# Kernel tuning notes

Measured on AMD Instinct MI355X. Metric: run time of the kernel, lower is better.

Reference implementation:

```python
import jax, jax.numpy as jnp
import numpy as np

VOCAB, EMBED, HIDDEN, NUM_OUT = 50000, 256, 64, 16
BATCH, T = 64, 2048
BN_EPS = 1e-5


def setup_inputs() -> dict:
    key = jax.random.key(0)
    ks = jax.random.split(key, 12)
    x = jax.random.randint(ks[0], (BATCH, T), 0, VOCAB, dtype=jnp.int64)
    seq_lengths = jax.random.randint(ks[1], (BATCH,), 1, T, dtype=jnp.int64)
    emb = jax.random.normal(ks[2], (VOCAB, EMBED), dtype=jnp.float32) * 0.1
    emb = emb.at[0].set(0.0)  # padding_idx=0
    s_ih = 1.0 / np.sqrt(HIDDEN)
    W_ih = jax.random.uniform(ks[3], (4 * HIDDEN, EMBED), jnp.float32, -s_ih, s_ih)
    W_hh = jax.random.uniform(ks[4], (4 * HIDDEN, HIDDEN), jnp.float32, -s_ih, s_ih)
    b_ih = jax.random.uniform(ks[5], (4 * HIDDEN,), jnp.float32, -s_ih, s_ih)
    b_hh = jax.random.uniform(ks[6], (4 * HIDDEN,), jnp.float32, -s_ih, s_ih)
    bn_gamma = jnp.ones((HIDDEN,), jnp.float32)
    bn_beta = jnp.zeros((HIDDEN,), jnp.float32)
    bn_mean = jnp.zeros((HIDDEN,), jnp.float32)
    bn_var = jnp.ones((HIDDEN,), jnp.float32)
    s_fc = 1.0 / np.sqrt(HIDDEN)
    fc_w = jax.random.uniform(ks[7], (NUM_OUT, HIDDEN), jnp.float32, -s_fc, s_fc)
    fc_b = jax.random.uniform(ks[8], (NUM_OUT,), jnp.float32, -s_fc, s_fc)
    return {"x": x, "seq_lengths": seq_lengths, "emb": emb, "W_ih": W_ih,
            "W_hh": W_hh, "b_ih": b_ih, "b_hh": b_hh, "bn_gamma": bn_gamma,
            "bn_beta": bn_beta, "bn_mean": bn_mean, "bn_var": bn_var,
            "fc_w": fc_w, "fc_b": fc_b}


def reference(x, seq_lengths, emb, W_ih, W_hh, b_ih, b_hh,
              bn_gamma, bn_beta, bn_mean, bn_var, fc_w, fc_b):
    B, Tn = x.shape
    H = W_hh.shape[1]
    x_embed = emb[x]                       # [B, T, E] (dropout is identity in eval)
    xe_t = jnp.transpose(x_embed, (1, 0, 2))  # [T, B, E] time-major for scan
    # precompute input projections for all timesteps in one big GEMM
    gx = jnp.einsum('tbe,ge->tbg', xe_t, W_ih) + b_ih + b_hh  # [T, B, 4H]

    def step(carry, gxt):
        h, c = carry
        gates = gxt + h @ W_hh.T           # [B, 4H]
        i, f, g, o = jnp.split(gates, 4, axis=-1)  # torch LSTMCell gate order
        i = jax.nn.sigmoid(i)
        f = jax.nn.sigmoid(f)
        g = jnp.tanh(g)
        o = jax.nn.sigmoid(o)
        c = f * c + i * g
        h = o * jnp.tanh(c)
        return (h, c), None

    h0 = jnp.zeros((B, H), x_embed.dtype)
    c0 = jnp.zeros((B, H), x_embed.dtype)
    (h_last, _), _ = jax.lax.scan(step, (h0, c0), gx)
    # BatchNorm1d (eval mode: running stats)
    h_bn = (h_last - bn_mean) * jax.lax.rsqrt(bn_var + BN_EPS) * bn_gamma + bn_beta
    return h_bn @ fc_w.T + fc_b            # [B, num_output]
```

## Files before the change

### kernel.cpp

```cpp
#include <hip/hip_runtime.h>
#include <math.h>

#define VOCAB   50000
#define EMBED   256
#define HIDDEN  64
#define G4      256
#define BATCH   64
#define TSEQ    2048
#define NUM_OUT 16

typedef _Float16 h2    __attribute__((ext_vector_type(2)));
typedef _Float16 f16x8 __attribute__((ext_vector_type(8)));
typedef float    f32x4 __attribute__((ext_vector_type(4)));

#define LOG2E  1.4426950408889634f
#define LOG2E2 2.8853900817779268f

__device__ __forceinline__ float fexp2f(float x) { return __builtin_amdgcn_exp2f(x); }
__device__ __forceinline__ float frcpf(float x)  { return __builtin_amdgcn_rcpf(x); }

__device__ __forceinline__ float dot2(h2 a, h2 b, float c) {
#if __has_builtin(__builtin_amdgcn_fdot2)
    return __builtin_amdgcn_fdot2(a, b, c, false);
#else
    float r;
    asm("v_dot2_f32_f16 %0, %1, %2, %3"
        : "=v"(r)
        : "v"(__builtin_bit_cast(int, a)), "v"(__builtin_bit_cast(int, b)), "v"(c));
    return r;
#endif
}

template <int CTRL>
__device__ __forceinline__ float dppf(float v) {
    return __int_as_float(__builtin_amdgcn_update_dpp(
        0, __float_as_int(v), CTRL, 0xF, 0xF, true));
}

#define REP32(M) M(0) M(1) M(2) M(3) M(4) M(5) M(6) M(7) \
                 M(8) M(9) M(10) M(11) M(12) M(13) M(14) M(15) \
                 M(16) M(17) M(18) M(19) M(20) M(21) M(22) M(23) \
                 M(24) M(25) M(26) M(27) M(28) M(29) M(30) M(31)

__device__ __align__(16) short g_Wf16[G4 * EMBED];

__global__ __launch_bounds__(256) void wcvt_kernel(const float* __restrict__ W_ih) {
    int i = (blockIdx.x * 256 + threadIdx.x) * 4;
    float4 v = *(const float4*)&W_ih[i];
    short4 o;
    o.x = __builtin_bit_cast(short, (_Float16)v.x);
    o.y = __builtin_bit_cast(short, (_Float16)v.y);
    o.z = __builtin_bit_cast(short, (_Float16)v.z);
    o.w = __builtin_bit_cast(short, (_Float16)v.w);
    *(short4*)&g_Wf16[i] = o;
}

__global__ __launch_bounds__(256) void proj_mfma(
    const float* __restrict__ emb,
    const float* __restrict__ b_ih, const float* __restrict__ b_hh,
    float* __restrict__ proj)
{
    __shared__ __align__(16) short As[64][264];

    const int tid  = threadIdx.x;
    const int w    = tid >> 6;
    const int lane = tid & 63;
    const int R0   = blockIdx.x * 64;

    #pragma unroll
    for (int it = 0; it < 16; ++it) {
        int flat = it * 256 + tid;
        int r  = flat >> 6;
        int c4 = flat & 63;
        int row = R0 + r; row = row < VOCAB ? row : VOCAB - 1;
        float4 v = *(const float4*)&emb[(size_t)row * EMBED + c4 * 4];
        short4 o;
        o.x = __builtin_bit_cast(short, (_Float16)v.x);
        o.y = __builtin_bit_cast(short, (_Float16)v.y);
        o.z = __builtin_bit_cast(short, (_Float16)v.z);
        o.w = __builtin_bit_cast(short, (_Float16)v.w);
        *(short4*)&As[r][c4 * 4] = o;
    }
    __syncthreads();

    f32x4 acc[16];
    #pragma unroll
    for (int t = 0; t < 16; ++t) acc[t] = f32x4{0.f, 0.f, 0.f, 0.f};

    const short* arow = &As[w * 16 + (lane & 15)][(lane >> 4) * 8];
    const int boff = (lane & 15) * EMBED + (lane >> 4) * 8;

    #pragma unroll
    for (int kc = 0; kc < 8; ++kc) {
        f16x8 af = *(const f16x8*)(arow + kc * 32);
        #pragma unroll
        for (int t = 0; t < 16; ++t) {
            f16x8 bf = *(const f16x8*)&g_Wf16[t * 16 * EMBED + kc * 32 + boff];
            acc[t] = __builtin_amdgcn_mfma_f32_16x16x32_f16(af, bf, acc[t], 0, 0, 0);
        }
    }

    const int crow0 = R0 + w * 16 + (lane >> 4) * 4;
    const int colin = lane & 15;
    #pragma unroll
    for (int t = 0; t < 16; ++t) {
        int g = t * 16 + colin;
        float bias = b_ih[g] + b_hh[g];
        float sc = ((g >> 6) == 2) ? LOG2E2 : LOG2E;
        #pragma unroll
        for (int j = 0; j < 4; ++j) {
            int row = crow0 + j;
            if (row < VOCAB)
                proj[(size_t)row * G4 + g] = (acc[t][j] + bias) * sc;
        }
    }
}

__global__ __launch_bounds__(256) void lstm_scan(
    const int* __restrict__ x, const float* __restrict__ proj,
    const float* __restrict__ W_hh,
    const float* __restrict__ bn_gamma, const float* __restrict__ bn_beta,
    const float* __restrict__ bn_mean, const float* __restrict__ bn_var,
    const float* __restrict__ fc_w, const float* __restrict__ fc_b,
    float* __restrict__ out)
{
    const int b   = blockIdx.x;
    const int tid = threadIdx.x;
    const int w   = tid >> 6;
    const int l   = tid & 63;
    const int q   = l & 3;
    const int unit = w * 16 + (l >> 2);

    __shared__ int   toks[TSEQ + 8];
    __shared__ __align__(16) short hbuf[2][HIDDEN];
    __shared__ float hfin[HIDDEN];
    __shared__ float hb_s[HIDDEN];

    for (int i = tid; i < TSEQ + 8; i += 256)
        toks[i] = x[b * TSEQ + (i < TSEQ ? i : TSEQ - 1)];
    if (tid < 2 * HIDDEN) ((short*)hbuf)[tid] = 0;

    const float s_k = (q == 2) ? LOG2E2 : LOG2E;
    const float* Wr = &W_hh[(size_t)(q * HIDDEN + unit) * HIDDEN];
#define WR_DECL(n) h2 wr##n;
    REP32(WR_DECL)
#undef WR_DECL
#define WR_LOAD(n) { float2 v = *(const float2*)&Wr[2 * (n)]; \
                     wr##n = h2{(_Float16)(v.x * s_k), (_Float16)(v.y * s_k)}; }
    REP32(WR_LOAD)
#undef WR_LOAD

    const float s_c = (q == 2) ? LOG2E2 : 1.0f;
    const float s_m = (q == 2) ? 2.0f * LOG2E2 : 1.0f;
    const bool qodd = (q & 1) != 0;
    const bool qhi  = (q & 2) != 0;

    float c = 0.0f, hmy = 0.0f;
    const float* projw = proj + q * HIDDEN + unit;

    __syncthreads();

    float gx0 = projw[(size_t)toks[0] * G4];
    float gx1 = projw[(size_t)toks[1] * G4];
    float gx2 = projw[(size_t)toks[2] * G4];
    float gx3 = projw[(size_t)toks[3] * G4];
    int tk0 = toks[4], tk1 = toks[5], tk2 = toks[6], tk3 = toks[7];

    const int4* hp0 = (const int4*)hbuf[0];
    const int4* hp1 = (const int4*)hbuf[1];

#define DOTG(R, W0, W1, W2, W3) \
    a0 = dot2(W0, __builtin_bit_cast(h2, R.x), a0); \
    a1 = dot2(W1, __builtin_bit_cast(h2, R.y), a1); \
    a2 = dot2(W2, __builtin_bit_cast(h2, R.z), a2); \
    a3 = dot2(W3, __builtin_bit_cast(h2, R.w), a3);

#define STEP(HP, WB, GX, TK, TT) { \
    int4 r0 = (HP)[0], r1 = (HP)[1], r2 = (HP)[2], r3 = (HP)[3]; \
    int4 r4 = (HP)[4], r5 = (HP)[5], r6 = (HP)[6], r7 = (HP)[7]; \
    int tnew = toks[(TT) + 8]; \
    float gnew = projw[(size_t)(TK) * G4]; \
    float a0 = GX, a1 = 0.f, a2 = 0.f, a3 = 0.f; \
    DOTG(r0, wr0,  wr1,  wr2,  wr3)  DOTG(r1, wr4,  wr5,  wr6,  wr7) \
    DOTG(r2, wr8,  wr9,  wr10, wr11) DOTG(r3, wr12, wr13, wr14, wr15) \
    DOTG(r4, wr16, wr17, wr18, wr19) DOTG(r5, wr20, wr21, wr22, wr23) \
    DOTG(r6, wr24, wr25, wr26, wr27) DOTG(r7, wr28, wr29, wr30, wr31) \
    float gv = (a0 + a1) + (a2 + a3); \
    GX = gnew; TK = tnew; \
    float tt2 = fexp2f(gv); \
    float rr = fmaf(-s_m, frcpf(tt2 + 1.0f), s_c);        \
    float b1 = dppf<0xB1>(rr);                            \
    float b2 = dppf<0x4E>(rr);                            \
    float b3 = dppf<0x1B>(rr);                            \
    float A  = qodd ? b1 : rr,  B  = qodd ? b3 : b2; \
    float A2 = qodd ? rr : b1,  B2 = qodd ? b2 : b3; \
    float i_ = qhi ? B  : A,    g_ = qhi ? A  : B; \
    float f_ = qhi ? B2 : A2,   o_ = qhi ? A2 : B2; \
    float o2 = o_ + o_; \
    c = fmaf(f_, c, i_ * g_);                             \
    float e2 = fexp2f(c); \
    float rv = frcpf(e2 + 1.0f); \
    hmy = fmaf(-o2, rv, o_);                              \
    if (q == 0) hbuf[WB][unit] = __builtin_bit_cast(short, (_Float16)hmy); \
    asm volatile("s_waitcnt lgkmcnt(0)" ::: "memory"); \
    __builtin_amdgcn_s_barrier(); \
    asm volatile("" ::: "memory"); \
}

    for (int t = 0; t < TSEQ; t += 4) {
        STEP(hp0, 1, gx0, tk0, t)
        STEP(hp1, 0, gx1, tk1, t + 1)
        STEP(hp0, 1, gx2, tk2, t + 2)
        STEP(hp1, 0, gx3, tk3, t + 3)
    }
#undef STEP
#undef DOTG

    if (q == 0) hfin[unit] = hmy;
    __syncthreads();
    if (tid < HIDDEN) {
        float hb = (hfin[tid] - bn_mean[tid]) * rsqrtf(bn_var[tid] + 1e-5f)
                   * bn_gamma[tid] + bn_beta[tid];
        hb_s[tid] = hb;
    }
    __syncthreads();
    if (tid < NUM_OUT) {
        float s0 = fc_b[tid], s1 = 0.f, s2 = 0.f, s3 = 0.f;
        #pragma unroll
        for (int k = 0; k < HIDDEN; k += 4) {
            s0 = fmaf(hb_s[k + 0], fc_w[tid * HIDDEN + k + 0], s0);
            s1 = fmaf(hb_s[k + 1], fc_w[tid * HIDDEN + k + 1], s1);
            s2 = fmaf(hb_s[k + 2], fc_w[tid * HIDDEN + k + 2], s2);
            s3 = fmaf(hb_s[k + 3], fc_w[tid * HIDDEN + k + 3], s3);
        }
        out[b * NUM_OUT + tid] = (s0 + s1) + (s2 + s3);
    }
}

extern "C" void kernel_launch(void* const* d_in, const int* in_sizes, int n_in,
                              void* d_out, int out_size, void* d_ws, size_t ws_size,
                              hipStream_t stream) {
    const int*   x        = (const int*)d_in[0];
    const float* emb      = (const float*)d_in[2];
    const float* W_ih     = (const float*)d_in[3];
    const float* W_hh     = (const float*)d_in[4];
    const float* b_ih     = (const float*)d_in[5];
    const float* b_hh     = (const float*)d_in[6];
    const float* bn_gamma = (const float*)d_in[7];
    const float* bn_beta  = (const float*)d_in[8];
    const float* bn_mean  = (const float*)d_in[9];
    const float* bn_var   = (const float*)d_in[10];
    const float* fc_w     = (const float*)d_in[11];
    const float* fc_b     = (const float*)d_in[12];

    float* proj = (float*)d_ws;

    wcvt_kernel<<<G4 * EMBED / (256 * 4), 256, 0, stream>>>(W_ih);
    proj_mfma<<<(VOCAB + 63) / 64, 256, 0, stream>>>(emb, b_ih, b_hh, proj);

    lstm_scan<<<BATCH, 256, 0, stream>>>(x, proj, W_hh,
                                         bn_gamma, bn_beta, bn_mean, bn_var,
                                         fc_w, fc_b, (float*)d_out);
}
```

Baseline: 642.6 us.

## Run LSTM recurrence in a single wavefront using MFMA for the hidden matmul

The per-batch scan kernel moves from 256 threads with fp16 dot2 products and a block barrier every step to a single 64-lane wavefront. That wavefront computes h·W_hh^T with 16x16x32 MFMA instructions, W_hh is kept in registers as f16 B fragments, and h is exchanged through a small shared buffer with no s_barrier. The projection table layout is permuted so each lane can fetch its 16 gate inputs with four float4 loads, and the projection kernel writes vectorized float4 stores. The aim is to remove the cross-wave barrier cost and the latency of the dot-product chain on the serial critical path. In exchange, most MFMA output is wasted because only row 0 is used, and each lane must compute 16 activations per step.

```diff
diff --git a/kernel.cpp b/kernel.cpp
--- a/kernel.cpp
+++ b/kernel.cpp
@@ -9,7 +9,6 @@
 #define TSEQ    2048
 #define NUM_OUT 16
 
-typedef _Float16 h2    __attribute__((ext_vector_type(2)));
 typedef _Float16 f16x8 __attribute__((ext_vector_type(8)));
 typedef float    f32x4 __attribute__((ext_vector_type(4)));
 
@@ -19,28 +18,17 @@
 __device__ __forceinline__ float fexp2f(float x) { return __builtin_amdgcn_exp2f(x); }
 __device__ __forceinline__ float frcpf(float x)  { return __builtin_amdgcn_rcpf(x); }
 
-__device__ __forceinline__ float dot2(h2 a, h2 b, float c) {
-#if __has_builtin(__builtin_amdgcn_fdot2)
-    return __builtin_amdgcn_fdot2(a, b, c, false);
-#else
-    float r;
-    asm("v_dot2_f32_f16 %0, %1, %2, %3"
-        : "=v"(r)
-        : "v"(__builtin_bit_cast(int, a)), "v"(__builtin_bit_cast(int, b)), "v"(c));
-    return r;
-#endif
-}
-
-template <int CTRL>
-__device__ __forceinline__ float dppf(float v) {
-    return __int_as_float(__builtin_amdgcn_update_dpp(
-        0, __float_as_int(v), CTRL, 0xF, 0xF, true));
-}
-
-#define REP32(M) M(0) M(1) M(2) M(3) M(4) M(5) M(6) M(7) \
-                 M(8) M(9) M(10) M(11) M(12) M(13) M(14) M(15) \
-                 M(16) M(17) M(18) M(19) M(20) M(21) M(22) M(23) \
-                 M(24) M(25) M(26) M(27) M(28) M(29) M(30) M(31)
+__device__ __forceinline__ int dpp_xor1(int v) {
+    return __builtin_amdgcn_update_dpp(0, v, 0xB1, 0xF, 0xF, true);
+}
+__device__ __forceinline__ int pkpair(float h) {
+    int hp = dpp_xor1(__float_as_int(h));
+    return __builtin_bit_cast(int,
+        __builtin_amdgcn_cvt_pkrtz(h, __int_as_float(hp)));
+}
+
+#define REP16(M) M(0) M(1) M(2) M(3) M(4) M(5) M(6) M(7) \
+                 M(8) M(9) M(10) M(11) M(12) M(13) M(14) M(15)
 
 __device__ __align__(16) short g_Wf16[G4 * EMBED];
 
@@ -102,21 +90,33 @@
 
     const int crow0 = R0 + w * 16 + (lane >> 4) * 4;
     const int colin = lane & 15;
+
+    float bs[16], sc[16];
     #pragma unroll
     for (int t = 0; t < 16; ++t) {
         int g = t * 16 + colin;
-        float bias = b_ih[g] + b_hh[g];
-        float sc = ((g >> 6) == 2) ? LOG2E2 : LOG2E;
-        #pragma unroll
-        for (int j = 0; j < 4; ++j) {
-            int row = crow0 + j;
-            if (row < VOCAB)
-                proj[(size_t)row * G4 + g] = (acc[t][j] + bias) * sc;
-        }
-    }
-}
-
-__global__ __launch_bounds__(256) void lstm_scan(
+        bs[t] = b_ih[g] + b_hh[g];
+        sc[t] = ((t >> 2) == 2) ? LOG2E2 : LOG2E;
+    }
+
+    #pragma unroll
+    for (int j = 0; j < 4; ++j) {
+        int row = crow0 + j;
+        if (row < VOCAB) {
+            #pragma unroll
+            for (int a = 0; a < 4; ++a) {
+                float4 o;
+                o.x = (acc[4 * a + 0][j] + bs[4 * a + 0]) * sc[4 * a + 0];
+                o.y = (acc[4 * a + 1][j] + bs[4 * a + 1]) * sc[4 * a + 1];
+                o.z = (acc[4 * a + 2][j] + bs[4 * a + 2]) * sc[4 * a + 2];
+                o.w = (acc[4 * a + 3][j] + bs[4 * a + 3]) * sc[4 * a + 3];
+                *(float4*)&proj[(size_t)row * G4 + colin * 16 + 4 * a] = o;
+            }
+        }
+    }
+}
+
+__global__ __launch_bounds__(64, 1) void lstm_scan(
     const int* __restrict__ x, const float* __restrict__ proj,
     const float* __restrict__ W_hh,
     const float* __restrict__ bn_gamma, const float* __restrict__ bn_beta,
@@ -124,116 +124,134 @@
     const float* __restrict__ fc_w, const float* __restrict__ fc_b,
     float* __restrict__ out)
 {
-    const int b   = blockIdx.x;
-    const int tid = threadIdx.x;
-    const int w   = tid >> 6;
-    const int l   = tid & 63;
-    const int q   = l & 3;
-    const int unit = w * 16 + (l >> 2);
-
-    __shared__ int   toks[TSEQ + 8];
-    __shared__ __align__(16) short hbuf[2][HIDDEN];
-    __shared__ float hfin[HIDDEN];
+    const int b    = blockIdx.x;
+    const int lane = threadIdx.x;
+    const int g    = lane >> 4;
+    const int c    = lane & 15;
+
+    __shared__ int   toks[TSEQ + 4];
+    __shared__ __align__(16) int hx[32];
     __shared__ float hb_s[HIDDEN];
 
-    for (int i = tid; i < TSEQ + 8; i += 256)
+    for (int i = lane; i < TSEQ + 4; i += 64)
         toks[i] = x[b * TSEQ + (i < TSEQ ? i : TSEQ - 1)];
-    if (tid < 2 * HIDDEN) ((short*)hbuf)[tid] = 0;
-
-    const float s_k = (q == 2) ? LOG2E2 : LOG2E;
-    const float* Wr = &W_hh[(size_t)(q * HIDDEN + unit) * HIDDEN];
-#define WR_DECL(n) h2 wr##n;
-    REP32(WR_DECL)
-#undef WR_DECL
-#define WR_LOAD(n) { float2 v = *(const float2*)&Wr[2 * (n)]; \
-                     wr##n = h2{(_Float16)(v.x * s_k), (_Float16)(v.y * s_k)}; }
-    REP32(WR_LOAD)
-#undef WR_LOAD
-
-    const float s_c = (q == 2) ? LOG2E2 : 1.0f;
-    const float s_m = (q == 2) ? 2.0f * LOG2E2 : 1.0f;
-    const bool qodd = (q & 1) != 0;
-    const bool qhi  = (q & 2) != 0;
-
-    float c = 0.0f, hmy = 0.0f;
-    const float* projw = proj + q * HIDDEN + unit;
-
-    __syncthreads();
-
-    float gx0 = projw[(size_t)toks[0] * G4];
-    float gx1 = projw[(size_t)toks[1] * G4];
-    float gx2 = projw[(size_t)toks[2] * G4];
-    float gx3 = projw[(size_t)toks[3] * G4];
-    int tk0 = toks[4], tk1 = toks[5], tk2 = toks[6], tk3 = toks[7];
-
-    const int4* hp0 = (const int4*)hbuf[0];
-    const int4* hp1 = (const int4*)hbuf[1];
-
-#define DOTG(R, W0, W1, W2, W3) \
-    a0 = dot2(W0, __builtin_bit_cast(h2, R.x), a0); \
-    a1 = dot2(W1, __builtin_bit_cast(h2, R.y), a1); \
-    a2 = dot2(W2, __builtin_bit_cast(h2, R.z), a2); \
-    a3 = dot2(W3, __builtin_bit_cast(h2, R.w), a3);
-
-#define STEP(HP, WB, GX, TK, TT) { \
-    int4 r0 = (HP)[0], r1 = (HP)[1], r2 = (HP)[2], r3 = (HP)[3]; \
-    int4 r4 = (HP)[4], r5 = (HP)[5], r6 = (HP)[6], r7 = (HP)[7]; \
-    int tnew = toks[(TT) + 8]; \
-    float gnew = projw[(size_t)(TK) * G4]; \
-    float a0 = GX, a1 = 0.f, a2 = 0.f, a3 = 0.f; \
-    DOTG(r0, wr0,  wr1,  wr2,  wr3)  DOTG(r1, wr4,  wr5,  wr6,  wr7) \
-    DOTG(r2, wr8,  wr9,  wr10, wr11) DOTG(r3, wr12, wr13, wr14, wr15) \
-    DOTG(r4, wr16, wr17, wr18, wr19) DOTG(r5, wr20, wr21, wr22, wr23) \
-    DOTG(r6, wr24, wr25, wr26, wr27) DOTG(r7, wr28, wr29, wr30, wr31) \
-    float gv = (a0 + a1) + (a2 + a3); \
-    GX = gnew; TK = tnew; \
-    float tt2 = fexp2f(gv); \
-    float rr = fmaf(-s_m, frcpf(tt2 + 1.0f), s_c);        \
-    float b1 = dppf<0xB1>(rr);                            \
-    float b2 = dppf<0x4E>(rr);                            \
-    float b3 = dppf<0x1B>(rr);                            \
-    float A  = qodd ? b1 : rr,  B  = qodd ? b3 : b2; \
-    float A2 = qodd ? rr : b1,  B2 = qodd ? b2 : b3; \
-    float i_ = qhi ? B  : A,    g_ = qhi ? A  : B; \
-    float f_ = qhi ? B2 : A2,   o_ = qhi ? A2 : B2; \
-    float o2 = o_ + o_; \
-    c = fmaf(f_, c, i_ * g_);                             \
-    float e2 = fexp2f(c); \
-    float rv = frcpf(e2 + 1.0f); \
-    hmy = fmaf(-o2, rv, o_);                              \
-    if (q == 0) hbuf[WB][unit] = __builtin_bit_cast(short, (_Float16)hmy); \
-    asm volatile("s_waitcnt lgkmcnt(0)" ::: "memory"); \
-    __builtin_amdgcn_s_barrier(); \
-    asm volatile("" ::: "memory"); \
-}
-
-    for (int t = 0; t < TSEQ; t += 4) {
-        STEP(hp0, 1, gx0, tk0, t)
-        STEP(hp1, 0, gx1, tk1, t + 1)
-        STEP(hp0, 1, gx2, tk2, t + 2)
-        STEP(hp1, 0, gx3, tk3, t + 3)
+    if (lane < 32) hx[lane] = 0;
+
+#define BDECL(t) f16x8 Ba##t, Bb##t;
+    REP16(BDECL)
+#undef BDECL
+#define BLOAD(t) { \
+        const float* wr = W_hh + (size_t)(t * 16 + c) * HIDDEN + g * 8; \
+        const float sck = ((t >> 2) == 2) ? LOG2E2 : LOG2E; \
+        float4 lo = *(const float4*)wr; \
+        float4 hi = *(const float4*)(wr + 4); \
+        Ba##t = f16x8{(_Float16)(lo.x*sck), (_Float16)(lo.y*sck), \
+                      (_Float16)(lo.z*sck), (_Float16)(lo.w*sck), \
+                      (_Float16)(hi.x*sck), (_Float16)(hi.y*sck), \
+                      (_Float16)(hi.z*sck), (_Float16)(hi.w*sck)}; \
+        lo = *(const float4*)(wr + 32); \
+        hi = *(const float4*)(wr + 36); \
+        Bb##t = f16x8{(_Float16)(lo.x*sck), (_Float16)(lo.y*sck), \
+                      (_Float16)(lo.z*sck), (_Float16)(lo.w*sck), \
+                      (_Float16)(hi.x*sck), (_Float16)(hi.y*sck), \
+                      (_Float16)(hi.z*sck), (_Float16)(hi.w*sck)}; }
+    REP16(BLOAD)
+#undef BLOAD
+
+    float cc0 = 0.f, cc1 = 0.f, cc2 = 0.f, cc3 = 0.f;
+    float hs0 = 0.f, hs1 = 0.f, hs2 = 0.f, hs3 = 0.f;
+
+    const float* projc = proj + c * 16;
+
+    const float4* gp0 = (const float4*)(projc + (size_t)toks[0] * G4);
+    const float4* gp1 = (const float4*)(projc + (size_t)toks[1] * G4);
+    float4 P0 = gp0[0], P1 = gp0[1], P2 = gp0[2], P3 = gp0[3];
+    float4 R0 = gp1[0], R1 = gp1[1], R2 = gp1[2], R3 = gp1[3];
+
+#define STEP(Q0, Q1, Q2, Q3, TT) { \
+    const int4* hx4 = (const int4*)hx; \
+    int4 a0i = hx4[g]; \
+    int4 a1i = hx4[4 + g]; \
+    f16x8 A0 = __builtin_bit_cast(f16x8, a0i); \
+    f16x8 A1 = __builtin_bit_cast(f16x8, a1i); \
+    int tk = toks[(TT) + 2]; \
+    const float4* gp = (const float4*)(projc + (size_t)tk * G4); \
+    float4 n0 = gp[0], n1 = gp[1], n2 = gp[2], n3 = gp[3]; \
+    float gxv[16]; \
+    gxv[0]=Q0.x; gxv[1]=Q0.y; gxv[2]=Q0.z; gxv[3]=Q0.w; \
+    gxv[4]=Q1.x; gxv[5]=Q1.y; gxv[6]=Q1.z; gxv[7]=Q1.w; \
+    gxv[8]=Q2.x; gxv[9]=Q2.y; gxv[10]=Q2.z; gxv[11]=Q2.w; \
+    gxv[12]=Q3.x; gxv[13]=Q3.y; gxv[14]=Q3.z; gxv[15]=Q3.w; \
+    const f32x4 zz = {0.f, 0.f, 0.f, 0.f}; \
+    MFMAS(A0, A1, zz) \
+    ACTS() \
+    UPD(0, r0, r4, r8,  r12) \
+    UPD(1, r1, r5, r9,  r13) \
+    UPD(2, r2, r6, r10, r14) \
+    UPD(3, r3, r7, r11, r15) \
+    int pk0 = pkpair(hs0), pk1 = pkpair(hs1); \
+    int pk2 = pkpair(hs2), pk3 = pkpair(hs3); \
+    if ((lane & 0x31) == 0) { \
+        int bi = c >> 1; \
+        hx[bi] = pk0; hx[8 + bi] = pk1; \
+        hx[16 + bi] = pk2; hx[24 + bi] = pk3; \
+    } \
+    Q0 = n0; Q1 = n1; Q2 = n2; Q3 = n3; \
+}
+#define MFMA1(t, A0, A1, ZZ) \
+    f32x4 ac##t = __builtin_amdgcn_mfma_f32_16x16x32_f16(A0, Ba##t, ZZ, 0, 0, 0); \
+    ac##t = __builtin_amdgcn_mfma_f32_16x16x32_f16(A1, Bb##t, ac##t, 0, 0, 0);
+#define MFMAS(A0, A1, ZZ) \
+    MFMA1(0,A0,A1,ZZ)  MFMA1(1,A0,A1,ZZ)  MFMA1(2,A0,A1,ZZ)  MFMA1(3,A0,A1,ZZ) \
+    MFMA1(4,A0,A1,ZZ)  MFMA1(5,A0,A1,ZZ)  MFMA1(6,A0,A1,ZZ)  MFMA1(7,A0,A1,ZZ) \
+    MFMA1(8,A0,A1,ZZ)  MFMA1(9,A0,A1,ZZ)  MFMA1(10,A0,A1,ZZ) MFMA1(11,A0,A1,ZZ) \
+    MFMA1(12,A0,A1,ZZ) MFMA1(13,A0,A1,ZZ) MFMA1(14,A0,A1,ZZ) MFMA1(15,A0,A1,ZZ)
+#define ACT1(t) float r##t; { \
+    float gv = ac##t[0] + gxv[t]; \
+    float e  = fexp2f(gv); \
+    float rv = frcpf(e + 1.0f); \
+    r##t = ((t) >> 2) == 2 ? fmaf(-2.0f * LOG2E2, rv, LOG2E2) \
+                           : fmaf(-1.0f, rv, 1.0f); }
+#define ACTS() \
+    ACT1(0)  ACT1(1)  ACT1(2)  ACT1(3)  ACT1(4)  ACT1(5)  ACT1(6)  ACT1(7) \
+    ACT1(8)  ACT1(9)  ACT1(10) ACT1(11) ACT1(12) ACT1(13) ACT1(14) ACT1(15)
+#define UPD(s, RI, RF, RG, RO) { \
+    cc##s = fmaf(RF, cc##s, RI * RG); \
+    float e2 = fexp2f(cc##s); \
+    float rv2 = frcpf(e2 + 1.0f); \
+    hs##s = fmaf(-(RO + RO), rv2, RO); }
+
+    for (int t = 0; t < TSEQ; t += 2) {
+        STEP(P0, P1, P2, P3, t)
+        STEP(R0, R1, R2, R3, t + 1)
     }
 #undef STEP
-#undef DOTG
-
-    if (q == 0) hfin[unit] = hmy;
-    __syncthreads();
-    if (tid < HIDDEN) {
-        float hb = (hfin[tid] - bn_mean[tid]) * rsqrtf(bn_var[tid] + 1e-5f)
-                   * bn_gamma[tid] + bn_beta[tid];
-        hb_s[tid] = hb;
-    }
-    __syncthreads();
-    if (tid < NUM_OUT) {
-        float s0 = fc_b[tid], s1 = 0.f, s2 = 0.f, s3 = 0.f;
+#undef MFMAS
+#undef MFMA1
+#undef ACTS
+#undef ACT1
+#undef UPD
+
+    if ((lane & 48) == 0) {
+        float hv[4] = {hs0, hs1, hs2, hs3};
+        #pragma unroll
+        for (int s = 0; s < 4; ++s) {
+            int u = 16 * s + c;
+            float hb = (hv[s] - bn_mean[u]) * rsqrtf(bn_var[u] + 1e-5f)
+                       * bn_gamma[u] + bn_beta[u];
+            hb_s[u] = hb;
+        }
+    }
+    if (lane < NUM_OUT) {
+        float s0 = fc_b[lane], s1 = 0.f, s2 = 0.f, s3 = 0.f;
         #pragma unroll
         for (int k = 0; k < HIDDEN; k += 4) {
-            s0 = fmaf(hb_s[k + 0], fc_w[tid * HIDDEN + k + 0], s0);
-            s1 = fmaf(hb_s[k + 1], fc_w[tid * HIDDEN + k + 1], s1);
-            s2 = fmaf(hb_s[k + 2], fc_w[tid * HIDDEN + k + 2], s2);
-            s3 = fmaf(hb_s[k + 3], fc_w[tid * HIDDEN + k + 3], s3);
-        }
-        out[b * NUM_OUT + tid] = (s0 + s1) + (s2 + s3);
+            s0 = fmaf(hb_s[k + 0], fc_w[lane * HIDDEN + k + 0], s0);
+            s1 = fmaf(hb_s[k + 1], fc_w[lane * HIDDEN + k + 1], s1);
+            s2 = fmaf(hb_s[k + 2], fc_w[lane * HIDDEN + k + 2], s2);
+            s3 = fmaf(hb_s[k + 3], fc_w[lane * HIDDEN + k + 3], s3);
+        }
+        out[b * NUM_OUT + lane] = (s0 + s1) + (s2 + s3);
     }
 }
 
@@ -258,7 +276,7 @@
     wcvt_kernel<<<G4 * EMBED / (256 * 4), 256, 0, stream>>>(W_ih);
     proj_mfma<<<(VOCAB + 63) / 64, 256, 0, stream>>>(emb, b_ih, b_hh, proj);
 
-    lstm_scan<<<BATCH, 256, 0, stream>>>(x, proj, W_hh,
-                                         bn_gamma, bn_beta, bn_mean, bn_var,
-                                         fc_w, fc_b, (float*)d_out);
-}
+    lstm_scan<<<BATCH, 64, 0, stream>>>(x, proj, W_hh,
+                                        bn_gamma, bn_beta, bn_mean, bn_var,
+                                        fc_w, fc_b, (float*)d_out);
+}
```

Result: slower. 1.246 ms (+93.9%).

## Run LSTM recurrence in one wavefront per batch with LDS-resident weights

Applied to the files above, without the earlier changes.

The scan kernel drops from four waves per batch to a single 64-thread wave. Each thread now computes all four gates of one hidden unit, reading fp16 recurrent weights from LDS and sharing h through a packed fp16 LDS buffer. This removes the per-timestep cross-wave barrier and the DPP gate shuffles. The projection table is rewritten so each unit's four gates sit together and load as one float4. The trade-off is four times more dot products per thread, plus large per-step LDS weight reads that now sit on the serial critical path.

```diff
diff --git a/kernel.cpp b/kernel.cpp
--- a/kernel.cpp
+++ b/kernel.cpp
@@ -31,16 +31,15 @@
 #endif
 }
 
-template <int CTRL>
-__device__ __forceinline__ float dppf(float v) {
-    return __int_as_float(__builtin_amdgcn_update_dpp(
-        0, __float_as_int(v), CTRL, 0xF, 0xF, true));
-}
-
-#define REP32(M) M(0) M(1) M(2) M(3) M(4) M(5) M(6) M(7) \
-                 M(8) M(9) M(10) M(11) M(12) M(13) M(14) M(15) \
-                 M(16) M(17) M(18) M(19) M(20) M(21) M(22) M(23) \
-                 M(24) M(25) M(26) M(27) M(28) M(29) M(30) M(31)
+__device__ __forceinline__ int dpp_xor1(int v) {
+    return __builtin_amdgcn_update_dpp(0, v, 0xB1, 0xF, 0xF, true);
+}
+__device__ __forceinline__ int pkpair(float h) {
+    int hp = dpp_xor1(__float_as_int(h));
+    return __builtin_bit_cast(int,
+        __builtin_amdgcn_cvt_pkrtz(h, __int_as_float(hp)));
+}
+__device__ __forceinline__ h2 bch2(int v) { return __builtin_bit_cast(h2, v); }
 
 __device__ __align__(16) short g_Wf16[G4 * EMBED];
 
@@ -102,21 +101,34 @@
 
     const int crow0 = R0 + w * 16 + (lane >> 4) * 4;
     const int colin = lane & 15;
-    #pragma unroll
-    for (int t = 0; t < 16; ++t) {
-        int g = t * 16 + colin;
-        float bias = b_ih[g] + b_hh[g];
-        float sc = ((g >> 6) == 2) ? LOG2E2 : LOG2E;
-        #pragma unroll
-        for (int j = 0; j < 4; ++j) {
-            int row = crow0 + j;
-            if (row < VOCAB)
-                proj[(size_t)row * G4 + g] = (acc[t][j] + bias) * sc;
-        }
-    }
-}
-
-__global__ __launch_bounds__(256) void lstm_scan(
+
+    float bs[4][4];
+    #pragma unroll
+    for (int q = 0; q < 4; ++q)
+        #pragma unroll
+        for (int ug = 0; ug < 4; ++ug) {
+            int gidx = q * 64 + ug * 16 + colin;
+            bs[q][ug] = b_ih[gidx] + b_hh[gidx];
+        }
+
+    #pragma unroll
+    for (int j = 0; j < 4; ++j) {
+        int row = crow0 + j;
+        if (row < VOCAB) {
+            #pragma unroll
+            for (int ug = 0; ug < 4; ++ug) {
+                float4 o;
+                o.x = (acc[0 * 4 + ug][j] + bs[0][ug]) * LOG2E;
+                o.y = (acc[1 * 4 + ug][j] + bs[1][ug]) * LOG2E;
+                o.z = (acc[2 * 4 + ug][j] + bs[2][ug]) * LOG2E2;
+                o.w = (acc[3 * 4 + ug][j] + bs[3][ug]) * LOG2E;
+                *(float4*)&proj[(size_t)row * G4 + (ug * 16 + colin) * 4] = o;
+            }
+        }
+    }
+}
+
+__global__ __launch_bounds__(64) void lstm_scan(
     const int* __restrict__ x, const float* __restrict__ proj,
     const float* __restrict__ W_hh,
     const float* __restrict__ bn_gamma, const float* __restrict__ bn_beta,
@@ -124,116 +136,109 @@
     const float* __restrict__ fc_w, const float* __restrict__ fc_b,
     float* __restrict__ out)
 {
-    const int b   = blockIdx.x;
-    const int tid = threadIdx.x;
-    const int w   = tid >> 6;
-    const int l   = tid & 63;
-    const int q   = l & 3;
-    const int unit = w * 16 + (l >> 2);
+    const int b = blockIdx.x;
+    const int j = threadIdx.x;
 
     __shared__ int   toks[TSEQ + 8];
-    __shared__ __align__(16) short hbuf[2][HIDDEN];
-    __shared__ float hfin[HIDDEN];
+    __shared__ __align__(16) short wlds[32 * 64 * 8];
+    __shared__ __align__(16) int   hx[32];
     __shared__ float hb_s[HIDDEN];
 
-    for (int i = tid; i < TSEQ + 8; i += 256)
+    for (int i = j; i < TSEQ + 8; i += 64)
         toks[i] = x[b * TSEQ + (i < TSEQ ? i : TSEQ - 1)];
-    if (tid < 2 * HIDDEN) ((short*)hbuf)[tid] = 0;
-
-    const float s_k = (q == 2) ? LOG2E2 : LOG2E;
-    const float* Wr = &W_hh[(size_t)(q * HIDDEN + unit) * HIDDEN];
-#define WR_DECL(n) h2 wr##n;
-    REP32(WR_DECL)
-#undef WR_DECL
-#define WR_LOAD(n) { float2 v = *(const float2*)&Wr[2 * (n)]; \
-                     wr##n = h2{(_Float16)(v.x * s_k), (_Float16)(v.y * s_k)}; }
-    REP32(WR_LOAD)
-#undef WR_LOAD
-
-    const float s_c = (q == 2) ? LOG2E2 : 1.0f;
-    const float s_m = (q == 2) ? 2.0f * LOG2E2 : 1.0f;
-    const bool qodd = (q & 1) != 0;
-    const bool qhi  = (q & 2) != 0;
-
-    float c = 0.0f, hmy = 0.0f;
-    const float* projw = proj + q * HIDDEN + unit;
-
+    if (j < 32) hx[j] = 0;
+
+    #pragma unroll
+    for (int q = 0; q < 4; ++q) {
+        const float* wr = W_hh + (size_t)(q * HIDDEN + j) * HIDDEN;
+        const float sck = (q == 2) ? LOG2E2 : LOG2E;
+        #pragma unroll
+        for (int m = 0; m < 8; ++m) {
+            float4 lo = *(const float4*)(wr + m * 8);
+            float4 hi = *(const float4*)(wr + m * 8 + 4);
+            int4 o;
+            o.x = __builtin_bit_cast(int, h2{(_Float16)(lo.x * sck), (_Float16)(lo.y * sck)});
+            o.y = __builtin_bit_cast(int, h2{(_Float16)(lo.z * sck), (_Float16)(lo.w * sck)});
+            o.z = __builtin_bit_cast(int, h2{(_Float16)(hi.x * sck), (_Float16)(hi.y * sck)});
+            o.w = __builtin_bit_cast(int, h2{(_Float16)(hi.z * sck), (_Float16)(hi.w * sck)});
+            *(int4*)&wlds[((m * 4 + q) * 64 + j) * 8] = o;
+        }
+    }
     __syncthreads();
 
-    float gx0 = projw[(size_t)toks[0] * G4];
-    float gx1 = projw[(size_t)toks[1] * G4];
-    float gx2 = projw[(size_t)toks[2] * G4];
-    float gx3 = projw[(size_t)toks[3] * G4];
+    float cc = 0.0f, hmy = 0.0f;
+    const float* projc = proj + j * 4;
+
+    float4 gx0 = *(const float4*)(projc + (size_t)toks[0] * G4);
+    float4 gx1 = *(const float4*)(projc + (size_t)toks[1] * G4);
+    float4 gx2 = *(const float4*)(projc + (size_t)toks[2] * G4);
+    float4 gx3 = *(const float4*)(projc + (size_t)toks[3] * G4);
     int tk0 = toks[4], tk1 = toks[5], tk2 = toks[6], tk3 = toks[7];
 
-    const int4* hp0 = (const int4*)hbuf[0];
-    const int4* hp1 = (const int4*)hbuf[1];
-
-#define DOTG(R, W0, W1, W2, W3) \
-    a0 = dot2(W0, __builtin_bit_cast(h2, R.x), a0); \
-    a1 = dot2(W1, __builtin_bit_cast(h2, R.y), a1); \
-    a2 = dot2(W2, __builtin_bit_cast(h2, R.z), a2); \
-    a3 = dot2(W3, __builtin_bit_cast(h2, R.w), a3);
-
-#define STEP(HP, WB, GX, TK, TT) { \
-    int4 r0 = (HP)[0], r1 = (HP)[1], r2 = (HP)[2], r3 = (HP)[3]; \
-    int4 r4 = (HP)[4], r5 = (HP)[5], r6 = (HP)[6], r7 = (HP)[7]; \
+#define GRP(m, R) { \
+    int4 w0 = wpj[((m) * 4 + 0) * 64]; \
+    int4 w1 = wpj[((m) * 4 + 1) * 64]; \
+    int4 w2 = wpj[((m) * 4 + 2) * 64]; \
+    int4 w3 = wpj[((m) * 4 + 3) * 64]; \
+    ai = dot2(bch2(w0.x), bch2(R.x), ai); ai = dot2(bch2(w0.y), bch2(R.y), ai); \
+    ai = dot2(bch2(w0.z), bch2(R.z), ai); ai = dot2(bch2(w0.w), bch2(R.w), ai); \
+    af = dot2(bch2(w1.x), bch2(R.x), af); af = dot2(bch2(w1.y), bch2(R.y), af); \
+    af = dot2(bch2(w1.z), bch2(R.z), af); af = dot2(bch2(w1.w), bch2(R.w), af); \
+    ag = dot2(bch2(w2.x), bch2(R.x), ag); ag = dot2(bch2(w2.y), bch2(R.y), ag); \
+    ag = dot2(bch2(w2.z), bch2(R.z), ag); ag = dot2(bch2(w2.w), bch2(R.w), ag); \
+    ao = dot2(bch2(w3.x), bch2(R.x), ao); ao = dot2(bch2(w3.y), bch2(R.y), ao); \
+    ao = dot2(bch2(w3.z), bch2(R.z), ao); ao = dot2(bch2(w3.w), bch2(R.w), ao); \
+}
+
+#define STEP(GX, TK, TT) { \
+     \
+    const int4* hp4 = (const int4*)hx; \
+    int4 r0 = hp4[0], r1 = hp4[1], r2 = hp4[2], r3 = hp4[3]; \
+    int4 r4 = hp4[4], r5 = hp4[5], r6 = hp4[6], r7 = hp4[7]; \
+     \
+    int woff = 0; \
+    asm volatile("" : "+v"(woff)); \
+    const int4* wpj = (const int4*)((const char*)wlds + woff) + j; \
     int tnew = toks[(TT) + 8]; \
-    float gnew = projw[(size_t)(TK) * G4]; \
-    float a0 = GX, a1 = 0.f, a2 = 0.f, a3 = 0.f; \
-    DOTG(r0, wr0,  wr1,  wr2,  wr3)  DOTG(r1, wr4,  wr5,  wr6,  wr7) \
-    DOTG(r2, wr8,  wr9,  wr10, wr11) DOTG(r3, wr12, wr13, wr14, wr15) \
-    DOTG(r4, wr16, wr17, wr18, wr19) DOTG(r5, wr20, wr21, wr22, wr23) \
-    DOTG(r6, wr24, wr25, wr26, wr27) DOTG(r7, wr28, wr29, wr30, wr31) \
-    float gv = (a0 + a1) + (a2 + a3); \
+    float4 gnew = *(const float4*)(projc + (size_t)(TK) * G4); \
+    float ai = GX.x, af = GX.y, ag = GX.z, ao = GX.w; \
+    GRP(0, r0) GRP(1, r1) GRP(2, r2) GRP(3, r3) \
+    GRP(4, r4) GRP(5, r5) GRP(6, r6) GRP(7, r7) \
     GX = gnew; TK = tnew; \
-    float tt2 = fexp2f(gv); \
-    float rr = fmaf(-s_m, frcpf(tt2 + 1.0f), s_c);        \
-    float b1 = dppf<0xB1>(rr);                            \
-    float b2 = dppf<0x4E>(rr);                            \
-    float b3 = dppf<0x1B>(rr);                            \
-    float A  = qodd ? b1 : rr,  B  = qodd ? b3 : b2; \
-    float A2 = qodd ? rr : b1,  B2 = qodd ? b2 : b3; \
-    float i_ = qhi ? B  : A,    g_ = qhi ? A  : B; \
-    float f_ = qhi ? B2 : A2,   o_ = qhi ? A2 : B2; \
-    float o2 = o_ + o_; \
-    c = fmaf(f_, c, i_ * g_);                             \
-    float e2 = fexp2f(c); \
-    float rv = frcpf(e2 + 1.0f); \
-    hmy = fmaf(-o2, rv, o_);                              \
-    if (q == 0) hbuf[WB][unit] = __builtin_bit_cast(short, (_Float16)hmy); \
-    asm volatile("s_waitcnt lgkmcnt(0)" ::: "memory"); \
-    __builtin_amdgcn_s_barrier(); \
-    asm volatile("" ::: "memory"); \
+    float i_ = 1.0f - frcpf(fexp2f(ai) + 1.0f); \
+    float f_ = 1.0f - frcpf(fexp2f(af) + 1.0f); \
+    float g_ = fmaf(-2.0f * LOG2E2, frcpf(fexp2f(ag) + 1.0f), LOG2E2); \
+    float o_ = 1.0f - frcpf(fexp2f(ao) + 1.0f); \
+    cc = fmaf(f_, cc, i_ * g_); \
+    float rv2 = frcpf(fexp2f(cc) + 1.0f); \
+    hmy = fmaf(-(o_ + o_), rv2, o_); \
+    int pk = pkpair(hmy); \
+    if ((j & 1) == 0) hx[j >> 1] = pk; \
 }
 
     for (int t = 0; t < TSEQ; t += 4) {
-        STEP(hp0, 1, gx0, tk0, t)
-        STEP(hp1, 0, gx1, tk1, t + 1)
-        STEP(hp0, 1, gx2, tk2, t + 2)
-        STEP(hp1, 0, gx3, tk3, t + 3)
+        STEP(gx0, tk0, t)
+        STEP(gx1, tk1, t + 1)
+        STEP(gx2, tk2, t + 2)
+        STEP(gx3, tk3, t + 3)
     }
 #undef STEP
-#undef DOTG
-
-    if (q == 0) hfin[unit] = hmy;
+#undef GRP
+
+    float hb = (hmy - bn_mean[j]) * rsqrtf(bn_var[j] + 1e-5f) * bn_gamma[j]
+               + bn_beta[j];
+    hb_s[j] = hb;
     __syncthreads();
-    if (tid < HIDDEN) {
-        float hb = (hfin[tid] - bn_mean[tid]) * rsqrtf(bn_var[tid] + 1e-5f)
-                   * bn_gamma[tid] + bn_beta[tid];
-        hb_s[tid] = hb;
-    }
-    __syncthreads();
-    if (tid < NUM_OUT) {
-        float s0 = fc_b[tid], s1 = 0.f, s2 = 0.f, s3 = 0.f;
+    if (j < NUM_OUT) {
+        float s0 = fc_b[j], s1 = 0.f, s2 = 0.f, s3 = 0.f;
         #pragma unroll
         for (int k = 0; k < HIDDEN; k += 4) {
-            s0 = fmaf(hb_s[k + 0], fc_w[tid * HIDDEN + k + 0], s0);
-            s1 = fmaf(hb_s[k + 1], fc_w[tid * HIDDEN + k + 1], s1);
-            s2 = fmaf(hb_s[k + 2], fc_w[tid * HIDDEN + k + 2], s2);
-            s3 = fmaf(hb_s[k + 3], fc_w[tid * HIDDEN + k + 3], s3);
-        }
-        out[b * NUM_OUT + tid] = (s0 + s1) + (s2 + s3);
+            s0 = fmaf(hb_s[k + 0], fc_w[j * HIDDEN + k + 0], s0);
+            s1 = fmaf(hb_s[k + 1], fc_w[j * HIDDEN + k + 1], s1);
+            s2 = fmaf(hb_s[k + 2], fc_w[j * HIDDEN + k + 2], s2);
+            s3 = fmaf(hb_s[k + 3], fc_w[j * HIDDEN + k + 3], s3);
+        }
+        out[b * NUM_OUT + j] = (s0 + s1) + (s2 + s3);
     }
 }
 
@@ -258,7 +263,7 @@
     wcvt_kernel<<<G4 * EMBED / (256 * 4), 256, 0, stream>>>(W_ih);
     proj_mfma<<<(VOCAB + 63) / 64, 256, 0, stream>>>(emb, b_ih, b_hh, proj);
 
-    lstm_scan<<<BATCH, 256, 0, stream>>>(x, proj, W_hh,
-                                         bn_gamma, bn_beta, bn_mean, bn_var,
-                                         fc_w, fc_b, (float*)d_out);
-}
+    lstm_scan<<<BATCH, 64, 0, stream>>>(x, proj, W_hh,
+                                        bn_gamma, bn_beta, bn_mean, bn_var,
+                                        fc_w, fc_b, (float*)d_out);
+}
```

Result: slower. 1.316 ms (+104.7%).
